# Optimization experiments

Hardware: AMD Instinct MI355X
Metric: run time of the kernel (lower is better)

Reference implementation:

```python
import jax, jax.numpy as jnp
import numpy as np

# Module hyperparameters (match init_kwargs)
S = 26          # grid size
NB = 3          # boxes per cell
C = 80          # num classes
LAMBDA_COORD = 5.0
LAMBDA_NOOBJ = 0.5
BATCH = 128
T = 50          # targets per image


def setup_inputs() -> dict:
    key = jax.random.key(0)
    k1, k2 = jax.random.split(key)
    predictions = jax.random.normal(k1, (BATCH, NB * (5 + C), S, S), dtype=jnp.float32)
    # targets[..., :] = (cls, cx, cy, w, h); rand in [0,1) -> all grid-valid, cls idx = 0
    targets = jax.random.uniform(k2, (BATCH, T, 5), dtype=jnp.float32)
    return {"predictions": predictions, "targets": targets}


def reference(predictions, targets):
    # [B, NB*(5+C), S, S] -> [B, S, S, NB, 5+C]
    p = predictions.transpose(0, 2, 3, 1).reshape(BATCH, S, S, NB, 5 + C)

    cls_f = targets[..., 0]
    cx, cy = targets[..., 1], targets[..., 2]
    w, h = targets[..., 3], targets[..., 4]

    gx = (cx * S).astype(jnp.int32)  # int() truncation; cx >= 0 so floor == trunc
    gy = (cy * S).astype(jnp.int32)
    valid = ((gx < S) & (gy < S)).astype(p.dtype)  # [BATCH, T]
    gxc = jnp.clip(gx, 0, S - 1)
    gyc = jnp.clip(gy, 0, S - 1)

    bidx = jnp.arange(BATCH)[:, None]  # [BATCH, 1]
    # gather responsible box 0 at each target's grid cell: [BATCH, T, 5+C]
    pb = p[bidx, gyc, gxc, 0]

    coord = ((pb[..., 1] - cx) ** 2 + (pb[..., 2] - cy) ** 2
             + (pb[..., 3] - w) ** 2 + (pb[..., 4] - h) ** 2)

    cls_idx = cls_f.astype(jnp.int32)
    one_hot = jax.nn.one_hot(cls_idx, C, dtype=p.dtype)  # [BATCH, T, C]
    cls_loss = jnp.sum((pb[..., 5:] - one_hot) ** 2, axis=-1)

    loss = jnp.sum(valid * (LAMBDA_COORD * coord + cls_loss))

    # object / no-object confidence masks via scatter (duplicates: set-to-1 is idempotent)
    obj = jnp.zeros((BATCH, S, S, NB), p.dtype).at[bidx, gyc, gxc, 0].max(valid)
    noobj = 1.0 - obj
    loss = loss + LAMBDA_NOOBJ * jnp.sum((p[..., 0] * noobj) ** 2)

    return loss / BATCH
```

## Files before the change

kernel.cpp:

```cpp
#include <hip/hip_runtime.h>

#define GS 26
#define NBOX 3
#define NCLS 80
#define BATCH 128
#define NTGT_PER 50
#define CELLS (GS * GS)
#define CHTOT (NBOX * (5 + NCLS))
#define NT (BATCH * NTGT_PER)
#define NCELL (BATCH * CELLS)
#define L_COORD 5.0f
#define L_NOOBJ 0.5f

__global__ void yolo_scatter_obj(const float* __restrict__ tgt,
                                 unsigned char* __restrict__ obj) {
    int t = blockIdx.x * blockDim.x + threadIdx.x;
    if (t >= NT) return;
    const float* tp = tgt + (size_t)t * 5;
    float cx = tp[1], cy = tp[2];
    int gx = (int)(cx * GS);
    int gy = (int)(cy * GS);
    if (gx < GS && gy < GS) {
        int gxc = min(max(gx, 0), GS - 1);
        int gyc = min(max(gy, 0), GS - 1);
        int b = t / NTGT_PER;
        obj[b * CELLS + gyc * GS + gxc] = 1;
    }
}

__global__ void yolo_loss(const float* __restrict__ pred,
                          const float* __restrict__ tgt,
                          const unsigned char* __restrict__ obj,
                          float* __restrict__ out) {
    int idx = blockIdx.x * blockDim.x + threadIdx.x;
    float acc = 0.0f;

    if (idx < NCELL) {
        int b = idx / CELLS;
        int cell = idx - b * CELLS;
        const float* base = pred + (size_t)b * CHTOT * CELLS + cell;
        float c0 = base[0];
        float c1 = base[(size_t)(1 * (5 + NCLS)) * CELLS];
        float c2 = base[(size_t)(2 * (5 + NCLS)) * CELLS];
        float no0 = obj[idx] ? 0.0f : 1.0f;
        acc += L_NOOBJ * (c0 * c0 * no0 + c1 * c1 + c2 * c2);
    }

    if (idx < NT) {
        const float* tp = tgt + (size_t)idx * 5;
        float cls = tp[0], cx = tp[1], cy = tp[2], w = tp[3], h = tp[4];
        int gx = (int)(cx * GS);
        int gy = (int)(cy * GS);
        if (gx < GS && gy < GS) {
            int gxc = min(max(gx, 0), GS - 1);
            int gyc = min(max(gy, 0), GS - 1);
            int b = idx / NTGT_PER;
            const float* pb = pred + (size_t)b * CHTOT * CELLS + gyc * GS + gxc;
            float d1 = pb[1 * CELLS] - cx;
            float d2 = pb[2 * CELLS] - cy;
            float d3 = pb[3 * CELLS] - w;
            float d4 = pb[4 * CELLS] - h;
            float coord = d1 * d1 + d2 * d2 + d3 * d3 + d4 * d4;
            int ci = (int)cls;
            float clsum = 0.0f;
            #pragma unroll
            for (int c = 0; c < NCLS; ++c) {
                float v = pb[(size_t)(5 + c) * CELLS] - ((c == ci) ? 1.0f : 0.0f);
                clsum += v * v;
            }
            acc += L_COORD * coord + clsum;
        }
    }

    #pragma unroll
    for (int off = 32; off > 0; off >>= 1)
        acc += __shfl_down(acc, off);
    __shared__ float ws[4];
    int lane = threadIdx.x & 63;
    int wid = threadIdx.x >> 6;
    if (lane == 0) ws[wid] = acc;
    __syncthreads();
    if (threadIdx.x == 0) {
        float v = ws[0] + ws[1] + ws[2] + ws[3];
        atomicAdd(out, v * (1.0f / BATCH));
    }
}

extern "C" void kernel_launch(void* const* d_in, const int* in_sizes, int n_in,
                              void* d_out, int out_size, void* d_ws, size_t ws_size,
                              hipStream_t stream) {
    const float* pred = (const float*)d_in[0];
    const float* tgt  = (const float*)d_in[1];
    float* out = (float*)d_out;
    unsigned char* obj = (unsigned char*)d_ws;

    hipMemsetAsync(obj, 0, NCELL, stream);
    hipMemsetAsync(out, 0, sizeof(float), stream);

    yolo_scatter_obj<<<(NT + 255) / 256, 256, 0, stream>>>(tgt, obj);

    int blocks = (NCELL + 255) / 256;
    yolo_loss<<<blocks, 256, 0, stream>>>(pred, tgt, obj, out);
}
```

Baseline: 142.9 us.

## Fuse obj scatter into per-image loss kernel with shared-memory mask

Replaces the workspace memset, the scatter kernel and the loss kernel with one kernel that handles one image per block. The objectness mask lives in shared memory, which removes two launches and the global mask traffic. Per-target class gathers are spread across the lanes of a wavefront instead of a serial 85-load loop in one thread. The trade-off is only 128 blocks, so parallelism is low on a GPU with many CUs.

```diff
diff --git a/kernel.cpp b/kernel.cpp
--- a/kernel.cpp
+++ b/kernel.cpp
@@ -6,82 +6,90 @@
 #define BATCH 128
 #define NTGT_PER 50
 #define CELLS (GS * GS)
-#define CHTOT (NBOX * (5 + NCLS))
-#define NT (BATCH * NTGT_PER)
-#define NCELL (BATCH * CELLS)
+#define CH (5 + NCLS)
+#define CHTOT (NBOX * CH)
 #define L_COORD 5.0f
 #define L_NOOBJ 0.5f
 
-__global__ void yolo_scatter_obj(const float* __restrict__ tgt,
-                                 unsigned char* __restrict__ obj) {
-    int t = blockIdx.x * blockDim.x + threadIdx.x;
-    if (t >= NT) return;
-    const float* tp = tgt + (size_t)t * 5;
-    float cx = tp[1], cy = tp[2];
-    int gx = (int)(cx * GS);
-    int gy = (int)(cy * GS);
-    if (gx < GS && gy < GS) {
-        int gxc = min(max(gx, 0), GS - 1);
-        int gyc = min(max(gy, 0), GS - 1);
-        int b = t / NTGT_PER;
-        obj[b * CELLS + gyc * GS + gxc] = 1;
-    }
-}
+__global__ __launch_bounds__(256) void yolo_fused(const float* __restrict__ pred,
+                                                  const float* __restrict__ tgt,
+                                                  float* __restrict__ out) {
+    const int b   = blockIdx.x;
+    const int tid = threadIdx.x;
 
-__global__ void yolo_loss(const float* __restrict__ pred,
-                          const float* __restrict__ tgt,
-                          const unsigned char* __restrict__ obj,
-                          float* __restrict__ out) {
-    int idx = blockIdx.x * blockDim.x + threadIdx.x;
-    float acc = 0.0f;
+    __shared__ float         stgt[NTGT_PER * 5];
+    __shared__ unsigned char obj[CELLS];
+    __shared__ float         wsum[4];
 
-    if (idx < NCELL) {
-        int b = idx / CELLS;
-        int cell = idx - b * CELLS;
-        const float* base = pred + (size_t)b * CHTOT * CELLS + cell;
-        float c0 = base[0];
-        float c1 = base[(size_t)(1 * (5 + NCLS)) * CELLS];
-        float c2 = base[(size_t)(2 * (5 + NCLS)) * CELLS];
-        float no0 = obj[idx] ? 0.0f : 1.0f;
-        acc += L_NOOBJ * (c0 * c0 * no0 + c1 * c1 + c2 * c2);
-    }
+    if (tid < NTGT_PER * 5) stgt[tid] = tgt[(size_t)b * NTGT_PER * 5 + tid];
+    for (int i = tid; i < CELLS; i += 256) obj[i] = 0;
+    __syncthreads();
 
-    if (idx < NT) {
-        const float* tp = tgt + (size_t)idx * 5;
-        float cls = tp[0], cx = tp[1], cy = tp[2], w = tp[3], h = tp[4];
+    if (tid < NTGT_PER) {
+        float cx = stgt[tid * 5 + 1], cy = stgt[tid * 5 + 2];
         int gx = (int)(cx * GS);
         int gy = (int)(cy * GS);
         if (gx < GS && gy < GS) {
             int gxc = min(max(gx, 0), GS - 1);
             int gyc = min(max(gy, 0), GS - 1);
-            int b = idx / NTGT_PER;
-            const float* pb = pred + (size_t)b * CHTOT * CELLS + gyc * GS + gxc;
-            float d1 = pb[1 * CELLS] - cx;
-            float d2 = pb[2 * CELLS] - cy;
-            float d3 = pb[3 * CELLS] - w;
-            float d4 = pb[4 * CELLS] - h;
-            float coord = d1 * d1 + d2 * d2 + d3 * d3 + d4 * d4;
-            int ci = (int)cls;
-            float clsum = 0.0f;
-            #pragma unroll
-            for (int c = 0; c < NCLS; ++c) {
-                float v = pb[(size_t)(5 + c) * CELLS] - ((c == ci) ? 1.0f : 0.0f);
-                clsum += v * v;
+            obj[gyc * GS + gxc] = 1;
+        }
+    }
+    __syncthreads();
+
+    float acc = 0.0f;
+    const float* pb0 = pred + (size_t)b * CHTOT * CELLS;
+
+    for (int cell = tid; cell < CELLS; cell += 256) {
+        float c0 = pb0[cell];
+        float c1 = pb0[(size_t)CH * CELLS + cell];
+        float c2 = pb0[(size_t)2 * CH * CELLS + cell];
+        float no0 = obj[cell] ? 0.0f : 1.0f;
+        acc += L_NOOBJ * (c0 * c0 * no0 + c1 * c1 + c2 * c2);
+    }
+
+    const int wid  = tid >> 6;
+    const int lane = tid & 63;
+    for (int t = wid; t < NTGT_PER; t += 4) {
+        float cls = stgt[t * 5 + 0];
+        float cx  = stgt[t * 5 + 1];
+        float cy  = stgt[t * 5 + 2];
+        float w   = stgt[t * 5 + 3];
+        float h   = stgt[t * 5 + 4];
+        int gx = (int)(cx * GS);
+        int gy = (int)(cy * GS);
+        if (gx >= GS || gy >= GS) continue;
+        int gxc = min(max(gx, 0), GS - 1);
+        int gyc = min(max(gy, 0), GS - 1);
+        int ci  = (int)cls;
+        const float* pb = pb0 + gyc * GS + gxc;
+
+        #pragma unroll
+        for (int rep = 0; rep < 2; ++rep) {
+            int j = lane + rep * 64;
+            if (j >= 1 && j < CH) {
+                float p = pb[(size_t)j * CELLS];
+                float tv, wgt;
+                if (j <= 4) {
+                    tv  = (j == 1) ? cx : (j == 2) ? cy : (j == 3) ? w : h;
+                    wgt = L_COORD;
+                } else {
+                    tv  = (j - 5 == ci) ? 1.0f : 0.0f;
+                    wgt = 1.0f;
+                }
+                float d = p - tv;
+                acc += wgt * d * d;
             }
-            acc += L_COORD * coord + clsum;
         }
     }
 
     #pragma unroll
     for (int off = 32; off > 0; off >>= 1)
         acc += __shfl_down(acc, off);
-    __shared__ float ws[4];
-    int lane = threadIdx.x & 63;
-    int wid = threadIdx.x >> 6;
-    if (lane == 0) ws[wid] = acc;
+    if (lane == 0) wsum[wid] = acc;
     __syncthreads();
-    if (threadIdx.x == 0) {
-        float v = ws[0] + ws[1] + ws[2] + ws[3];
+    if (tid == 0) {
+        float v = wsum[0] + wsum[1] + wsum[2] + wsum[3];
         atomicAdd(out, v * (1.0f / BATCH));
     }
 }
@@ -92,13 +100,7 @@
     const float* pred = (const float*)d_in[0];
     const float* tgt  = (const float*)d_in[1];
     float* out = (float*)d_out;
-    unsigned char* obj = (unsigned char*)d_ws;
 
-    hipMemsetAsync(obj, 0, NCELL, stream);
     hipMemsetAsync(out, 0, sizeof(float), stream);
-
-    yolo_scatter_obj<<<(NT + 255) / 256, 256, 0, stream>>>(tgt, obj);
-
-    int blocks = (NCELL + 255) / 256;
-    yolo_loss<<<blocks, 256, 0, stream>>>(pred, tgt, obj, out);
+    yolo_fused<<<BATCH, 256, 0, stream>>>(pred, tgt, out);
 }
```

Measured after the change: 129.6 us. 1.1x faster.
